# Performance work log

Measured on AMD Instinct MI355X. Metric: run time of the kernel, lower is better.

## Reference

```python
import jax, jax.numpy as jnp
import numpy as np

N, E, D = 100000, 1600000, 64
L = 3          # num_layers
EPS = 1e-5     # LayerNorm eps


def setup_inputs() -> dict:
    key = jax.random.key(0)
    ks = jax.random.split(key, 8)
    s = 0.05
    return {
        "x": jax.random.normal(ks[0], (N, D), jnp.float32),
        "edge_src": jax.random.randint(ks[1], (E,), 0, N, jnp.int32),
        "edge_dst": jax.random.randint(ks[2], (E,), 0, N, jnp.int32),
        # SAGEConv: lin_l (on aggregated neighbors, with bias), lin_r (root, no bias)
        "w_l": (jax.random.normal(ks[3], (L, D, D)) * s).astype(jnp.float32),
        "b_l": jnp.zeros((L, D), jnp.float32),
        "w_r": (jax.random.normal(ks[4], (L, D, D)) * s).astype(jnp.float32),
        # LayerNorm affine params per layer
        "gamma": jnp.ones((L, D), jnp.float32),
        "beta": jnp.zeros((L, D), jnp.float32),
        # residual projection (layer 0 only; Identity afterwards)
        "w_res": (jax.random.normal(ks[5], (D, D)) * s).astype(jnp.float32),
        "b_res": jnp.zeros((D,), jnp.float32),
        # final fc
        "w_fc": (jax.random.normal(ks[6], (D, D)) * s).astype(jnp.float32),
        "b_fc": jnp.zeros((D,), jnp.float32),
    }


def _layer_norm(h, g, b):
    mu = jnp.mean(h, axis=-1, keepdims=True)
    var = jnp.var(h, axis=-1, keepdims=True)
    return (h - mu) * jax.lax.rsqrt(var + EPS) * g + b


def reference(x, edge_src, edge_dst, w_l, b_l, w_r, gamma, beta, w_res, b_res, w_fc, b_fc):
    n = x.shape[0]
    # in-degree for mean aggregation (nodes with no in-edges get 0 aggregate)
    deg = jax.ops.segment_sum(jnp.ones(edge_dst.shape, x.dtype), edge_dst, num_segments=n)
    inv_deg = jnp.where(deg > 0, 1.0 / jnp.maximum(deg, 1.0), 0.0)[:, None]  # [N,1]
    for i in range(L):
        residual = x @ w_res + b_res if i == 0 else x
        # SAGEConv mean aggregation: gather source feats, scatter-sum at dst, divide by degree
        agg = jax.ops.segment_sum(x[edge_src], edge_dst, num_segments=n) * inv_deg  # [N,D]
        h = agg @ w_l[i] + b_l[i] + x @ w_r[i]
        h = jax.nn.relu(_layer_norm(h, gamma[i], beta[i]))
        # dropout is inactive in eval mode
        x = h + residual
    return x @ w_fc + b_fc
```

## Files before the change

### kernel.cpp

```cpp
#include <hip/hip_runtime.h>

typedef unsigned short u16;
typedef __bf16 bf16x8 __attribute__((ext_vector_type(8)));
typedef float f32x4 __attribute__((ext_vector_type(4)));

#define D 64
#define LPITCH 136
#define CHUNKS 256
#define BSHIFT 9

__device__ __forceinline__ float b2f(u16 u) {
    unsigned v = ((unsigned)u) << 16;
    float f;
    __builtin_memcpy(&f, &v, 4);
    return f;
}
__device__ __forceinline__ float u2f_lo(unsigned u) {
    unsigned v = u << 16;
    float f;
    __builtin_memcpy(&f, &v, 4);
    return f;
}
__device__ __forceinline__ float u2f_hi(unsigned u) {
    unsigned v = u & 0xFFFF0000u;
    float f;
    __builtin_memcpy(&f, &v, 4);
    return f;
}
__device__ __forceinline__ u16 f2b(float f) {
    unsigned u;
    __builtin_memcpy(&u, &f, 4);
    u = u + 0x7FFFu + ((u >> 16) & 1u);
    return (u16)(u >> 16);
}
__device__ __forceinline__ bf16x8 ld_frag(const u16* p) {
    union { uint4 u; bf16x8 b; } cv;
    cv.u = *(const uint4*)p;
    return cv.b;
}

__global__ __launch_bounds__(256) void binA_kernel(const int* __restrict__ dst, int E,
                                                   int* __restrict__ H,
                                                   int nbuck, int eper) {
    __shared__ int hist[256];
    int t = threadIdx.x;
    int c = blockIdx.x;
    hist[t] = 0;
    __syncthreads();
    int beg = c * eper;
    int end = min(beg + eper, E);
    for (int i = beg + t; i < end; i += 256) {
        atomicAdd(&hist[dst[i] >> BSHIFT], 1);
    }
    __syncthreads();
    if (t < nbuck) H[c * nbuck + t] = hist[t];
}

__global__ __launch_bounds__(256) void binS2_kernel(const int* __restrict__ H,
                                                    int* __restrict__ Orel,
                                                    int* __restrict__ T,
                                                    int nbuck) {
    __shared__ int ss[256];
    int b = blockIdx.x;
    int t = threadIdx.x;
    int h = H[t * nbuck + b];
    ss[t] = h;
    __syncthreads();
    for (int off = 1; off < 256; off <<= 1) {
        int v = (t >= off) ? ss[t - off] : 0;
        __syncthreads();
        ss[t] += v;
        __syncthreads();
    }
    Orel[t * nbuck + b] = ss[t] - h;
    if (t == 255) T[b] = ss[255];
}

__global__ __launch_bounds__(256) void binT_kernel(const int* __restrict__ T, int nbuck,
                                                   int* __restrict__ base,
                                                   int* __restrict__ row_ptr, int N) {
    __shared__ int sm[256];
    int t = threadIdx.x;
    int v = (t < nbuck) ? T[t] : 0;
    sm[t] = v;
    __syncthreads();
    for (int off = 1; off < 256; off <<= 1) {
        int u = (t >= off) ? sm[t - off] : 0;
        __syncthreads();
        sm[t] += u;
        __syncthreads();
    }
    if (t < nbuck) base[t] = sm[t] - v;
    if (t == 255) {
        base[nbuck] = sm[255];
        row_ptr[N] = sm[255];
    }
}

__global__ __launch_bounds__(256) void binB_kernel(const int* __restrict__ src,
                                                   const int* __restrict__ dst, int E,
                                                   const int* __restrict__ base,
                                                   const int* __restrict__ Orel,
                                                   int* __restrict__ staging,
                                                   int nbuck, int eper) {
    __shared__ int pos[256];
    int t = threadIdx.x;
    int c = blockIdx.x;
    if (t < nbuck) pos[t] = base[t] + Orel[c * nbuck + t];
    __syncthreads();
    int beg = c * eper;
    int end = min(beg + eper, E);
    const int mask = (1 << BSHIFT) - 1;
    for (int i = beg + t; i < end; i += 256) {
        int d = dst[i];
        int b = d >> BSHIFT;
        int p = atomicAdd(&pos[b], 1);
        staging[p] = src[i] | ((d & mask) << 17);
    }
}

__global__ __launch_bounds__(256) void binC_kernel(const int* __restrict__ staging,
                                                   const int* __restrict__ base,
                                                   int* __restrict__ row_ptr,
                                                   float* __restrict__ inv_deg,
                                                   int* __restrict__ col, int N) {
    __shared__ int cnt[512];
    __shared__ int lrp[512];
    __shared__ int sm[256];
    int b = blockIdx.x;
    int t = threadIdx.x;
    int node0 = b << BSHIFT;
    int nn = min(1 << BSHIFT, N - node0);
    cnt[t] = 0;
    cnt[t + 256] = 0;
    __syncthreads();
    int sbeg = base[b], send = base[b + 1];
    for (int i = sbeg + t; i < send; i += 256) {
        atomicAdd(&cnt[staging[i] >> 17], 1);
    }
    __syncthreads();
    int c0 = cnt[2 * t], c1 = cnt[2 * t + 1];
    sm[t] = c0 + c1;
    __syncthreads();
    for (int off = 1; off < 256; off <<= 1) {
        int v = (t >= off) ? sm[t - off] : 0;
        __syncthreads();
        sm[t] += v;
        __syncthreads();
    }
    int excl = sm[t] - c0 - c1;
    lrp[2 * t] = excl;
    lrp[2 * t + 1] = excl + c0;
    __syncthreads();
    for (int i = t; i < nn; i += 256) {
        row_ptr[node0 + i] = sbeg + lrp[i];
        int dd = cnt[i];
        inv_deg[node0 + i] = dd > 0 ? 1.0f / (float)dd : 0.0f;
    }
    __syncthreads();
    for (int i = sbeg + t; i < send; i += 256) {
        int word = staging[i];
        int ld = word >> 17;
        int k = atomicSub(&cnt[ld], 1) - 1;
        col[sbeg + lrp[ld] + k] = word & 0x1FFFF;
    }
}

__global__ __launch_bounds__(256) void cvtprep_kernel(const float* __restrict__ xf,
                                                      u16* __restrict__ xb, int total4,
                                                      const float* __restrict__ wl,
                                                      const float* __restrict__ wr,
                                                      const float* __restrict__ wres,
                                                      const float* __restrict__ wfc,
                                                      u16* __restrict__ WtL,
                                                      u16* __restrict__ WresT,
                                                      u16* __restrict__ WfcT) {
    int gid = blockIdx.x * 256 + threadIdx.x;
    int gstr = gridDim.x * 256;
    for (int i = gid; i < total4; i += gstr) {
        float4 v = *(const float4*)(xf + i * 4);
        ushort4 o;
        o.x = f2b(v.x); o.y = f2b(v.y); o.z = f2b(v.z); o.w = f2b(v.w);
        *(ushort4*)(xb + i * 4) = o;
    }
    for (int idx = gid; idx < 3 * 64 * 128; idx += gstr) {
        int l = idx >> 13;
        int rem = idx & 8191;
        int n = rem >> 7;
        int k = rem & 127;
        float v = (k < 64) ? wl[l * 4096 + k * 64 + n] : wr[l * 4096 + (k - 64) * 64 + n];
        WtL[idx] = f2b(v);
    }
    for (int idx = gid; idx < 4096; idx += gstr) {
        int n = idx >> 6, k = idx & 63;
        WresT[idx] = f2b(wres[k * 64 + n]);
        WfcT[idx] = f2b(wfc[k * 64 + n]);
    }
}

__global__ __launch_bounds__(256, 4) void layer_kernel(const u16* __restrict__ xb_in,
                                                       const int* __restrict__ row_ptr,
                                                       const int* __restrict__ col,
                                                       const float* __restrict__ inv_deg,
                                                       const u16* __restrict__ Wt,
                                                       const float* __restrict__ bl,
                                                       const float* __restrict__ gam,
                                                       const float* __restrict__ bet,
                                                       const u16* __restrict__ WresT,
                                                       const float* __restrict__ bres,
                                                       const u16* __restrict__ WfcT,
                                                       const float* __restrict__ bfc,
                                                       u16* __restrict__ xb_out,
                                                       float* __restrict__ fout,
                                                       int N, int layer0, int final_) {
    __shared__ __align__(16) u16 sA[64 * LPITCH];
    __shared__ __align__(16) u16 sB[64 * LPITCH];
    int tid = threadIdx.x;
    int base = blockIdx.x * 64;
    int lane = tid & 63;
    int w = tid >> 6;

#pragma unroll
    for (int i = 0; i < 4; i++) {
        int idx = i * 256 + tid;
        int r = idx >> 4, c = idx & 15;
        *(uint4*)&sB[r * LPITCH + c * 8] = *(const uint4*)(Wt + idx * 8);
    }
#pragma unroll
    for (int i = 0; i < 2; i++) {
        int idx = i * 256 + tid;
        int r = idx >> 3, c = idx & 7;
        int node = base + r;
        uint4 v = make_uint4(0, 0, 0, 0);
        if (node < N) v = *(const uint4*)(xb_in + node * D + c * 8);
        *(uint4*)&sA[r * LPITCH + 64 + c * 8] = v;
    }

    int slot = lane >> 3;
    int chunk = lane & 7;
#pragma unroll
    for (int r = 0; r < 2; r++) {
        int node_l = w * 16 + r * 8 + slot;
        int node = base + node_l;
        float a0 = 0, a1 = 0, a2 = 0, a3 = 0, a4 = 0, a5 = 0, a6 = 0, a7 = 0;
        uint4 o = make_uint4(0, 0, 0, 0);
        if (node < N) {
            int e = row_ptr[node], end = row_ptr[node + 1];
#define ACC(v)                                          \
    a0 += u2f_lo(v.x); a1 += u2f_hi(v.x);               \
    a2 += u2f_lo(v.y); a3 += u2f_hi(v.y);               \
    a4 += u2f_lo(v.z); a5 += u2f_hi(v.z);               \
    a6 += u2f_lo(v.w); a7 += u2f_hi(v.w);
            for (; e + 7 < end; e += 8) {
                int s0 = col[e],     s1 = col[e + 1], s2 = col[e + 2], s3 = col[e + 3];
                int s4 = col[e + 4], s5 = col[e + 5], s6 = col[e + 6], s7 = col[e + 7];
                uint4 v0 = *(const uint4*)(xb_in + s0 * D + chunk * 8);
                uint4 v1 = *(const uint4*)(xb_in + s1 * D + chunk * 8);
                uint4 v2 = *(const uint4*)(xb_in + s2 * D + chunk * 8);
                uint4 v3 = *(const uint4*)(xb_in + s3 * D + chunk * 8);
                uint4 v4 = *(const uint4*)(xb_in + s4 * D + chunk * 8);
                uint4 v5 = *(const uint4*)(xb_in + s5 * D + chunk * 8);
                uint4 v6 = *(const uint4*)(xb_in + s6 * D + chunk * 8);
                uint4 v7 = *(const uint4*)(xb_in + s7 * D + chunk * 8);
                ACC(v0) ACC(v1) ACC(v2) ACC(v3)
                ACC(v4) ACC(v5) ACC(v6) ACC(v7)
            }
            if (e + 3 < end) {
                int s0 = col[e], s1 = col[e + 1], s2 = col[e + 2], s3 = col[e + 3];
                uint4 v0 = *(const uint4*)(xb_in + s0 * D + chunk * 8);
                uint4 v1 = *(const uint4*)(xb_in + s1 * D + chunk * 8);
                uint4 v2 = *(const uint4*)(xb_in + s2 * D + chunk * 8);
                uint4 v3 = *(const uint4*)(xb_in + s3 * D + chunk * 8);
                ACC(v0) ACC(v1) ACC(v2) ACC(v3)
                e += 4;
            }
            if (e + 1 < end) {
                int s0 = col[e], s1 = col[e + 1];
                uint4 v0 = *(const uint4*)(xb_in + s0 * D + chunk * 8);
                uint4 v1 = *(const uint4*)(xb_in + s1 * D + chunk * 8);
                ACC(v0) ACC(v1)
                e += 2;
            }
            if (e < end) {
                int s0 = col[e];
                uint4 v0 = *(const uint4*)(xb_in + s0 * D + chunk * 8);
                ACC(v0)
            }
#undef ACC
            float m = inv_deg[node];
            o.x = (unsigned)f2b(a0 * m) | ((unsigned)f2b(a1 * m) << 16);
            o.y = (unsigned)f2b(a2 * m) | ((unsigned)f2b(a3 * m) << 16);
            o.z = (unsigned)f2b(a4 * m) | ((unsigned)f2b(a5 * m) << 16);
            o.w = (unsigned)f2b(a6 * m) | ((unsigned)f2b(a7 * m) << 16);
        }
        *(uint4*)&sA[node_l * LPITCH + chunk * 8] = o;
    }
    __syncthreads();

    int q = lane >> 4;
    int ln = lane & 15;
    f32x4 acc[4] = {{0, 0, 0, 0}, {0, 0, 0, 0}, {0, 0, 0, 0}, {0, 0, 0, 0}};
    f32x4 accr[4] = {{0, 0, 0, 0}, {0, 0, 0, 0}, {0, 0, 0, 0}, {0, 0, 0, 0}};
    const u16* aRow = &sA[(w * 16 + ln) * LPITCH];

#pragma unroll
    for (int c = 0; c < 4; c++) {
        bf16x8 a = ld_frag(&aRow[c * 32 + q * 8]);
#pragma unroll
        for (int t = 0; t < 4; t++) {
            bf16x8 b = ld_frag(&sB[(t * 16 + ln) * LPITCH + c * 32 + q * 8]);
            acc[t] = __builtin_amdgcn_mfma_f32_16x16x32_bf16(a, b, acc[t], 0, 0, 0);
        }
    }
    if (layer0) {
#pragma unroll
        for (int c = 0; c < 2; c++) {
            bf16x8 a = ld_frag(&aRow[64 + c * 32 + q * 8]);
#pragma unroll
            for (int t = 0; t < 4; t++) {
                bf16x8 b = ld_frag(WresT + (t * 16 + ln) * 64 + c * 32 + q * 8);
                accr[t] = __builtin_amdgcn_mfma_f32_16x16x32_bf16(a, b, accr[t], 0, 0, 0);
            }
        }
    }

    float bcol[4], gcol[4], btcol[4], brcol[4];
#pragma unroll
    for (int t = 0; t < 4; t++) {
        int colI = t * 16 + ln;
        bcol[t] = bl[colI];
        gcol[t] = gam[colI];
        btcol[t] = bet[colI];
        brcol[t] = layer0 ? bres[colI] : 0.f;
    }
#pragma unroll
    for (int t = 0; t < 4; t++)
#pragma unroll
        for (int r = 0; r < 4; r++) acc[t][r] += bcol[t];

    float ps[4], pq[4];
#pragma unroll
    for (int r = 0; r < 4; r++) {
        float s = 0, s2 = 0;
#pragma unroll
        for (int t = 0; t < 4; t++) { float h = acc[t][r]; s += h; s2 += h * h; }
        ps[r] = s; pq[r] = s2;
    }
    for (int off = 1; off < 16; off <<= 1) {
#pragma unroll
        for (int r = 0; r < 4; r++) {
            ps[r] += __shfl_xor(ps[r], off, 64);
            pq[r] += __shfl_xor(pq[r], off, 64);
        }
    }
#pragma unroll
    for (int r = 0; r < 4; r++) {
        int nb = w * 16 + q * 4 + r;
        float mu = ps[r] * (1.f / 64.f);
        float var = pq[r] * (1.f / 64.f) - mu * mu;
        var = var < 0.f ? 0.f : var;
        float rstd = rsqrtf(var + 1e-5f);
#pragma unroll
        for (int t = 0; t < 4; t++) {
            int colI = t * 16 + ln;
            float hn = (acc[t][r] - mu) * rstd * gcol[t] + btcol[t];
            hn = hn > 0.f ? hn : 0.f;
            float res = layer0 ? (accr[t][r] + brcol[t])
                               : b2f(sA[nb * LPITCH + 64 + colI]);
            sA[nb * LPITCH + colI] = f2b(hn + res);
        }
    }

    if (final_) {
        f32x4 accf[4] = {{0, 0, 0, 0}, {0, 0, 0, 0}, {0, 0, 0, 0}, {0, 0, 0, 0}};
#pragma unroll
        for (int c = 0; c < 2; c++) {
            bf16x8 a = ld_frag(&aRow[c * 32 + q * 8]);
#pragma unroll
            for (int t = 0; t < 4; t++) {
                bf16x8 b = ld_frag(WfcT + (t * 16 + ln) * 64 + c * 32 + q * 8);
                accf[t] = __builtin_amdgcn_mfma_f32_16x16x32_bf16(a, b, accf[t], 0, 0, 0);
            }
        }
#pragma unroll
        for (int r = 0; r < 4; r++) {
            int node = base + w * 16 + q * 4 + r;
            if (node >= N) continue;
#pragma unroll
            for (int t = 0; t < 4; t++) {
                int colI = t * 16 + ln;
                fout[node * D + colI] = accf[t][r] + bfc[colI];
            }
        }
    } else {
#pragma unroll
        for (int i = 0; i < 2; i++) {
            int idx = i * 64 + lane;
            int row = w * 16 + (idx >> 3);
            int ch = idx & 7;
            int node = base + row;
            if (node < N)
                *(uint4*)(xb_out + node * D + ch * 8) = *(const uint4*)&sA[row * LPITCH + ch * 8];
        }
    }
}

extern "C" void kernel_launch(void* const* d_in, const int* in_sizes, int n_in,
                              void* d_out, int out_size, void* d_ws, size_t ws_size,
                              hipStream_t stream) {
    const float* x_in = (const float*)d_in[0];
    const int* e_src = (const int*)d_in[1];
    const int* e_dst = (const int*)d_in[2];
    const float* w_l = (const float*)d_in[3];
    const float* b_l = (const float*)d_in[4];
    const float* w_r = (const float*)d_in[5];
    const float* gam = (const float*)d_in[6];
    const float* bet = (const float*)d_in[7];
    const float* w_res = (const float*)d_in[8];
    const float* b_res = (const float*)d_in[9];
    const float* w_fc = (const float*)d_in[10];
    const float* b_fc = (const float*)d_in[11];
    float* out = (float*)d_out;

    const int N = in_sizes[0] / D;
    const int E = in_sizes[1];
    const int nbuck = ((N - 1) >> BSHIFT) + 1;
    const int eper = (E + CHUNKS - 1) / CHUNKS;

    size_t o = 0;
    auto carve = [&](size_t bytes) {
        size_t cur = o;
        o += (bytes + 255) & ~(size_t)255;
        return (char*)d_ws + cur;
    };
    int* row_ptr = (int*)carve((size_t)(N + 1) * 4);
    float* inv_deg = (float*)carve((size_t)N * 4);
    int* colA = (int*)carve((size_t)E * 4);
    int* staging = (int*)carve((size_t)E * 4);
    int* Hh = (int*)carve((size_t)CHUNKS * nbuck * 4);
    int* Orel = (int*)carve((size_t)CHUNKS * nbuck * 4);
    int* Tb = (int*)carve((size_t)nbuck * 4);
    int* baseB = (int*)carve((size_t)(nbuck + 1) * 4);
    u16* WtL = (u16*)carve(3 * 64 * 128 * 2);
    u16* WresT = (u16*)carve(64 * 64 * 2);
    u16* WfcT = (u16*)carve(64 * 64 * 2);
    u16* xbA = (u16*)carve((size_t)N * D * 2);
    u16* xbB = (u16*)carve((size_t)N * D * 2);

    binA_kernel<<<CHUNKS, 256, 0, stream>>>(e_dst, E, Hh, nbuck, eper);
    binS2_kernel<<<nbuck, 256, 0, stream>>>(Hh, Orel, Tb, nbuck);
    binT_kernel<<<1, 256, 0, stream>>>(Tb, nbuck, baseB, row_ptr, N);
    binB_kernel<<<CHUNKS, 256, 0, stream>>>(e_src, e_dst, E, baseB, Orel, staging, nbuck, eper);
    binC_kernel<<<nbuck, 256, 0, stream>>>(staging, baseB, row_ptr, inv_deg, colA, N);

    cvtprep_kernel<<<1024, 256, 0, stream>>>(x_in, xbA, N * D / 4,
                                             w_l, w_r, w_res, w_fc, WtL, WresT, WfcT);

    int gridT = (N + 63) / 64;

    layer_kernel<<<gridT, 256, 0, stream>>>(xbA, row_ptr, colA, inv_deg, WtL,
                                            b_l, gam, bet, WresT, b_res,
                                            WfcT, b_fc, xbB, out, N, 1, 0);
    layer_kernel<<<gridT, 256, 0, stream>>>(xbB, row_ptr, colA, inv_deg, WtL + 8192,
                                            b_l + 64, gam + 64, bet + 64, WresT, b_res,
                                            WfcT, b_fc, xbA, out, N, 0, 0);
    layer_kernel<<<gridT, 256, 0, stream>>>(xbA, row_ptr, colA, inv_deg, WtL + 16384,
                                            b_l + 128, gam + 128, bet + 128, WresT, b_res,
                                            WfcT, b_fc, xbB, out, N, 0, 1);
}
```

Before: 282.5 us.

## Use 128-node tiles with 512 threads and dynamic LDS work queue for aggregation

Doubles the layer kernel tile to 128 nodes with 512 threads. Gather-aggregation slots now pull node indices from an LDS atomic counter, which balances uneven degrees across wavefronts. Row pointers and inverse degrees are staged in LDS first. The costs are an extra barrier, per-node atomics, and higher LDS use per block, which may limit occupancy.

```diff
diff --git a/kernel.cpp b/kernel.cpp
--- a/kernel.cpp
+++ b/kernel.cpp
@@ -6,6 +6,7 @@
 
 #define D 64
 #define LPITCH 136
+#define TILE 128
 #define CHUNKS 256
 #define BSHIFT 9
 
@@ -198,7 +199,7 @@
     }
 }
 
-__global__ __launch_bounds__(256, 4) void layer_kernel(const u16* __restrict__ xb_in,
+__global__ __launch_bounds__(512, 6) void layer_kernel(const u16* __restrict__ xb_in,
                                                        const int* __restrict__ row_ptr,
                                                        const int* __restrict__ col,
                                                        const float* __restrict__ inv_deg,
@@ -213,39 +214,50 @@
                                                        u16* __restrict__ xb_out,
                                                        float* __restrict__ fout,
                                                        int N, int layer0, int final_) {
-    __shared__ __align__(16) u16 sA[64 * LPITCH];
+    __shared__ __align__(16) u16 sA[TILE * LPITCH];
     __shared__ __align__(16) u16 sB[64 * LPITCH];
+    __shared__ int rp[TILE + 1];
+    __shared__ float ideg[TILE];
+    __shared__ int ctr;
     int tid = threadIdx.x;
-    int base = blockIdx.x * 64;
+    int base = blockIdx.x * TILE;
     int lane = tid & 63;
     int w = tid >> 6;
 
 #pragma unroll
-    for (int i = 0; i < 4; i++) {
-        int idx = i * 256 + tid;
+    for (int i = 0; i < 2; i++) {
+        int idx = i * 512 + tid;
         int r = idx >> 4, c = idx & 15;
         *(uint4*)&sB[r * LPITCH + c * 8] = *(const uint4*)(Wt + idx * 8);
     }
 #pragma unroll
     for (int i = 0; i < 2; i++) {
-        int idx = i * 256 + tid;
+        int idx = i * 512 + tid;
         int r = idx >> 3, c = idx & 7;
         int node = base + r;
         uint4 v = make_uint4(0, 0, 0, 0);
         if (node < N) v = *(const uint4*)(xb_in + node * D + c * 8);
         *(uint4*)&sA[r * LPITCH + 64 + c * 8] = v;
     }
-
-    int slot = lane >> 3;
+    if (tid <= TILE) {
+        int node = base + tid;
+        rp[tid] = (node <= N) ? row_ptr[node] : 0;
+        if (tid < TILE) ideg[tid] = (node < N) ? inv_deg[node] : 0.f;
+    }
+    if (tid == 0) ctr = 0;
+    __syncthreads();
+
     int chunk = lane & 7;
-#pragma unroll
-    for (int r = 0; r < 2; r++) {
-        int node_l = w * 16 + r * 8 + slot;
-        int node = base + node_l;
+    for (;;) {
+        int j = 0;
+        if ((lane & 7) == 0) j = atomicAdd(&ctr, 1);
+        j = __shfl(j, lane & 56, 64);
+        if (j >= TILE) break;
+        int node = base + j;
         float a0 = 0, a1 = 0, a2 = 0, a3 = 0, a4 = 0, a5 = 0, a6 = 0, a7 = 0;
         uint4 o = make_uint4(0, 0, 0, 0);
         if (node < N) {
-            int e = row_ptr[node], end = row_ptr[node + 1];
+            int e = rp[j], end = rp[j + 1];
 #define ACC(v)                                          \
     a0 += u2f_lo(v.x); a1 += u2f_hi(v.x);               \
     a2 += u2f_lo(v.y); a3 += u2f_hi(v.y);               \
@@ -287,13 +299,13 @@
                 ACC(v0)
             }
 #undef ACC
-            float m = inv_deg[node];
+            float m = ideg[j];
             o.x = (unsigned)f2b(a0 * m) | ((unsigned)f2b(a1 * m) << 16);
             o.y = (unsigned)f2b(a2 * m) | ((unsigned)f2b(a3 * m) << 16);
             o.z = (unsigned)f2b(a4 * m) | ((unsigned)f2b(a5 * m) << 16);
             o.w = (unsigned)f2b(a6 * m) | ((unsigned)f2b(a7 * m) << 16);
         }
-        *(uint4*)&sA[node_l * LPITCH + chunk * 8] = o;
+        *(uint4*)&sA[j * LPITCH + chunk * 8] = o;
     }
     __syncthreads();
 
@@ -456,15 +468,15 @@
     cvtprep_kernel<<<1024, 256, 0, stream>>>(x_in, xbA, N * D / 4,
                                              w_l, w_r, w_res, w_fc, WtL, WresT, WfcT);
 
-    int gridT = (N + 63) / 64;
-
-    layer_kernel<<<gridT, 256, 0, stream>>>(xbA, row_ptr, colA, inv_deg, WtL,
+    int gridT = (N + TILE - 1) / TILE;
+
+    layer_kernel<<<gridT, 512, 0, stream>>>(xbA, row_ptr, colA, inv_deg, WtL,
                                             b_l, gam, bet, WresT, b_res,
                                             WfcT, b_fc, xbB, out, N, 1, 0);
-    layer_kernel<<<gridT, 256, 0, stream>>>(xbB, row_ptr, colA, inv_deg, WtL + 8192,
+    layer_kernel<<<gridT, 512, 0, stream>>>(xbB, row_ptr, colA, inv_deg, WtL + 8192,
                                             b_l + 64, gam + 64, bet + 64, WresT, b_res,
                                             WfcT, b_fc, xbA, out, N, 0, 0);
-    layer_kernel<<<gridT, 256, 0, stream>>>(xbA, row_ptr, colA, inv_deg, WtL + 16384,
+    layer_kernel<<<gridT, 512, 0, stream>>>(xbA, row_ptr, colA, inv_deg, WtL + 16384,
                                             b_l + 128, gam + 128, bet + 128, WresT, b_res,
                                             WfcT, b_fc, xbB, out, N, 0, 1);
 }
```

Measured after the change: 318.8 us. +12.8%, slower.

## Merge CSR build and conversion kernels into one cooperative kernel

Applied to the files above, without the earlier changes.

Replaces the five CSR-binning kernels and the bf16 conversion kernel with a single cooperative launch of 256 blocks, using grid.sync() between phases. This removes five kernel launch boundaries and their drain/fill gaps, and lets the x/weight conversion run on the same grid after bucket sorting. In exchange it adds grid-wide barriers, and the conversion now runs on 256 blocks instead of 1024 and only after the CSR phases complete.

```diff
diff --git a/kernel.cpp b/kernel.cpp
--- a/kernel.cpp
+++ b/kernel.cpp
@@ -1,4 +1,7 @@
 #include <hip/hip_runtime.h>
+#include <hip/hip_cooperative_groups.h>
+
+namespace cg = cooperative_groups;
 
 typedef unsigned short u16;
 typedef __bf16 bf16x8 __attribute__((ext_vector_type(8)));
@@ -39,162 +42,156 @@
     return cv.b;
 }
 
-__global__ __launch_bounds__(256) void binA_kernel(const int* __restrict__ dst, int E,
-                                                   int* __restrict__ H,
-                                                   int nbuck, int eper) {
-    __shared__ int hist[256];
+struct CsrArgs {
+    const int* dst;
+    const int* src;
+    int E, N, nbuck, eper, total4;
+    int* H;
+    int* Orel;
+    int* T;
+    int* base;
+    int* row_ptr;
+    float* inv_deg;
+    int* staging;
+    int* col;
+    const float* xf;
+    const float* wl;
+    const float* wr;
+    const float* wres;
+    const float* wfc;
+    u16* xb;
+    u16* WtL;
+    u16* WresT;
+    u16* WfcT;
+};
+
+__global__ __launch_bounds__(256) void csr_kernel(CsrArgs a) {
+    __shared__ union {
+        int hist[256];
+        struct { int cnt[512]; int lrp[512]; int sm[256]; } c;
+    } sh;
+    cg::grid_group grid = cg::this_grid();
     int t = threadIdx.x;
     int c = blockIdx.x;
-    hist[t] = 0;
+
+    sh.hist[t] = 0;
     __syncthreads();
-    int beg = c * eper;
-    int end = min(beg + eper, E);
-    for (int i = beg + t; i < end; i += 256) {
-        atomicAdd(&hist[dst[i] >> BSHIFT], 1);
+    {
+        int beg = c * a.eper, end = min(beg + a.eper, a.E);
+        for (int i = beg + t; i < end; i += 256)
+            atomicAdd(&sh.hist[a.dst[i] >> BSHIFT], 1);
     }
     __syncthreads();
-    if (t < nbuck) H[c * nbuck + t] = hist[t];
-}
-
-__global__ __launch_bounds__(256) void binS2_kernel(const int* __restrict__ H,
-                                                    int* __restrict__ Orel,
-                                                    int* __restrict__ T,
-                                                    int nbuck) {
-    __shared__ int ss[256];
-    int b = blockIdx.x;
-    int t = threadIdx.x;
-    int h = H[t * nbuck + b];
-    ss[t] = h;
-    __syncthreads();
-    for (int off = 1; off < 256; off <<= 1) {
-        int v = (t >= off) ? ss[t - off] : 0;
-        __syncthreads();
-        ss[t] += v;
-        __syncthreads();
-    }
-    Orel[t * nbuck + b] = ss[t] - h;
-    if (t == 255) T[b] = ss[255];
-}
-
-__global__ __launch_bounds__(256) void binT_kernel(const int* __restrict__ T, int nbuck,
-                                                   int* __restrict__ base,
-                                                   int* __restrict__ row_ptr, int N) {
-    __shared__ int sm[256];
-    int t = threadIdx.x;
-    int v = (t < nbuck) ? T[t] : 0;
-    sm[t] = v;
-    __syncthreads();
-    for (int off = 1; off < 256; off <<= 1) {
-        int u = (t >= off) ? sm[t - off] : 0;
-        __syncthreads();
-        sm[t] += u;
-        __syncthreads();
-    }
-    if (t < nbuck) base[t] = sm[t] - v;
-    if (t == 255) {
-        base[nbuck] = sm[255];
-        row_ptr[N] = sm[255];
-    }
-}
-
-__global__ __launch_bounds__(256) void binB_kernel(const int* __restrict__ src,
-                                                   const int* __restrict__ dst, int E,
-                                                   const int* __restrict__ base,
-                                                   const int* __restrict__ Orel,
-                                                   int* __restrict__ staging,
-                                                   int nbuck, int eper) {
-    __shared__ int pos[256];
-    int t = threadIdx.x;
-    int c = blockIdx.x;
-    if (t < nbuck) pos[t] = base[t] + Orel[c * nbuck + t];
-    __syncthreads();
-    int beg = c * eper;
-    int end = min(beg + eper, E);
-    const int mask = (1 << BSHIFT) - 1;
-    for (int i = beg + t; i < end; i += 256) {
-        int d = dst[i];
-        int b = d >> BSHIFT;
-        int p = atomicAdd(&pos[b], 1);
-        staging[p] = src[i] | ((d & mask) << 17);
-    }
-}
-
-__global__ __launch_bounds__(256) void binC_kernel(const int* __restrict__ staging,
-                                                   const int* __restrict__ base,
-                                                   int* __restrict__ row_ptr,
-                                                   float* __restrict__ inv_deg,
-                                                   int* __restrict__ col, int N) {
-    __shared__ int cnt[512];
-    __shared__ int lrp[512];
-    __shared__ int sm[256];
-    int b = blockIdx.x;
-    int t = threadIdx.x;
-    int node0 = b << BSHIFT;
-    int nn = min(1 << BSHIFT, N - node0);
-    cnt[t] = 0;
-    cnt[t + 256] = 0;
-    __syncthreads();
-    int sbeg = base[b], send = base[b + 1];
-    for (int i = sbeg + t; i < send; i += 256) {
-        atomicAdd(&cnt[staging[i] >> 17], 1);
-    }
-    __syncthreads();
-    int c0 = cnt[2 * t], c1 = cnt[2 * t + 1];
-    sm[t] = c0 + c1;
-    __syncthreads();
-    for (int off = 1; off < 256; off <<= 1) {
-        int v = (t >= off) ? sm[t - off] : 0;
-        __syncthreads();
-        sm[t] += v;
-        __syncthreads();
-    }
-    int excl = sm[t] - c0 - c1;
-    lrp[2 * t] = excl;
-    lrp[2 * t + 1] = excl + c0;
-    __syncthreads();
-    for (int i = t; i < nn; i += 256) {
-        row_ptr[node0 + i] = sbeg + lrp[i];
-        int dd = cnt[i];
-        inv_deg[node0 + i] = dd > 0 ? 1.0f / (float)dd : 0.0f;
-    }
-    __syncthreads();
-    for (int i = sbeg + t; i < send; i += 256) {
-        int word = staging[i];
-        int ld = word >> 17;
-        int k = atomicSub(&cnt[ld], 1) - 1;
-        col[sbeg + lrp[ld] + k] = word & 0x1FFFF;
-    }
-}
-
-__global__ __launch_bounds__(256) void cvtprep_kernel(const float* __restrict__ xf,
-                                                      u16* __restrict__ xb, int total4,
-                                                      const float* __restrict__ wl,
-                                                      const float* __restrict__ wr,
-                                                      const float* __restrict__ wres,
-                                                      const float* __restrict__ wfc,
-                                                      u16* __restrict__ WtL,
-                                                      u16* __restrict__ WresT,
-                                                      u16* __restrict__ WfcT) {
-    int gid = blockIdx.x * 256 + threadIdx.x;
-    int gstr = gridDim.x * 256;
-    for (int i = gid; i < total4; i += gstr) {
-        float4 v = *(const float4*)(xf + i * 4);
-        ushort4 o;
-        o.x = f2b(v.x); o.y = f2b(v.y); o.z = f2b(v.z); o.w = f2b(v.w);
-        *(ushort4*)(xb + i * 4) = o;
-    }
-    for (int idx = gid; idx < 3 * 64 * 128; idx += gstr) {
-        int l = idx >> 13;
-        int rem = idx & 8191;
-        int n = rem >> 7;
-        int k = rem & 127;
-        float v = (k < 64) ? wl[l * 4096 + k * 64 + n] : wr[l * 4096 + (k - 64) * 64 + n];
-        WtL[idx] = f2b(v);
-    }
-    for (int idx = gid; idx < 4096; idx += gstr) {
-        int n = idx >> 6, k = idx & 63;
-        WresT[idx] = f2b(wres[k * 64 + n]);
-        WfcT[idx] = f2b(wfc[k * 64 + n]);
+    if (t < a.nbuck) a.H[c * a.nbuck + t] = sh.hist[t];
+    grid.sync();
+
+    if (c < a.nbuck) {
+        int h = a.H[t * a.nbuck + c];
+        sh.hist[t] = h;
+        __syncthreads();
+        for (int off = 1; off < 256; off <<= 1) {
+            int v = (t >= off) ? sh.hist[t - off] : 0;
+            __syncthreads();
+            sh.hist[t] += v;
+            __syncthreads();
+        }
+        a.Orel[t * a.nbuck + c] = sh.hist[t] - h;
+        if (t == 255) a.T[c] = sh.hist[255];
+    }
+    grid.sync();
+
+    if (c == 0) {
+        int v = (t < a.nbuck) ? a.T[t] : 0;
+        sh.hist[t] = v;
+        __syncthreads();
+        for (int off = 1; off < 256; off <<= 1) {
+            int u = (t >= off) ? sh.hist[t - off] : 0;
+            __syncthreads();
+            sh.hist[t] += u;
+            __syncthreads();
+        }
+        if (t < a.nbuck) a.base[t] = sh.hist[t] - v;
+        if (t == 255) {
+            a.base[a.nbuck] = sh.hist[255];
+            a.row_ptr[a.N] = sh.hist[255];
+        }
+    }
+    grid.sync();
+
+    {
+        if (t < a.nbuck) sh.hist[t] = a.base[t] + a.Orel[c * a.nbuck + t];
+        __syncthreads();
+        int beg = c * a.eper, end = min(beg + a.eper, a.E);
+        const int mask = (1 << BSHIFT) - 1;
+        for (int i = beg + t; i < end; i += 256) {
+            int d = a.dst[i];
+            int b = d >> BSHIFT;
+            int p = atomicAdd(&sh.hist[b], 1);
+            a.staging[p] = a.src[i] | ((d & mask) << 17);
+        }
+    }
+    grid.sync();
+
+    if (c < a.nbuck) {
+        int node0 = c << BSHIFT;
+        int nn = min(1 << BSHIFT, a.N - node0);
+        sh.c.cnt[t] = 0;
+        sh.c.cnt[t + 256] = 0;
+        __syncthreads();
+        int sbeg = a.base[c], send = a.base[c + 1];
+        for (int i = sbeg + t; i < send; i += 256)
+            atomicAdd(&sh.c.cnt[a.staging[i] >> 17], 1);
+        __syncthreads();
+        int c0 = sh.c.cnt[2 * t], c1 = sh.c.cnt[2 * t + 1];
+        sh.c.sm[t] = c0 + c1;
+        __syncthreads();
+        for (int off = 1; off < 256; off <<= 1) {
+            int v = (t >= off) ? sh.c.sm[t - off] : 0;
+            __syncthreads();
+            sh.c.sm[t] += v;
+            __syncthreads();
+        }
+        int excl = sh.c.sm[t] - c0 - c1;
+        sh.c.lrp[2 * t] = excl;
+        sh.c.lrp[2 * t + 1] = excl + c0;
+        __syncthreads();
+        for (int i = t; i < nn; i += 256) {
+            a.row_ptr[node0 + i] = sbeg + sh.c.lrp[i];
+            int dd = sh.c.cnt[i];
+            a.inv_deg[node0 + i] = dd > 0 ? 1.0f / (float)dd : 0.0f;
+        }
+        __syncthreads();
+        for (int i = sbeg + t; i < send; i += 256) {
+            int word = a.staging[i];
+            int ld = word >> 17;
+            int k = atomicSub(&sh.c.cnt[ld], 1) - 1;
+            a.col[sbeg + sh.c.lrp[ld] + k] = word & 0x1FFFF;
+        }
+    }
+
+    {
+        int gid = c * 256 + t;
+        int gstr = 256 * 256;
+        for (int i = gid; i < a.total4; i += gstr) {
+            float4 v = *(const float4*)(a.xf + i * 4);
+            ushort4 o;
+            o.x = f2b(v.x); o.y = f2b(v.y); o.z = f2b(v.z); o.w = f2b(v.w);
+            *(ushort4*)(a.xb + i * 4) = o;
+        }
+        for (int idx = gid; idx < 3 * 64 * 128; idx += gstr) {
+            int l = idx >> 13;
+            int rem = idx & 8191;
+            int n = rem >> 7;
+            int k = rem & 127;
+            float v = (k < 64) ? a.wl[l * 4096 + k * 64 + n]
+                               : a.wr[l * 4096 + (k - 64) * 64 + n];
+            a.WtL[idx] = f2b(v);
+        }
+        for (int idx = gid; idx < 4096; idx += gstr) {
+            int n = idx >> 6, k = idx & 63;
+            a.WresT[idx] = f2b(a.wres[k * 64 + n]);
+            a.WfcT[idx] = f2b(a.wfc[k * 64 + n]);
+        }
     }
 }
 
@@ -447,14 +444,34 @@
     u16* xbA = (u16*)carve((size_t)N * D * 2);
     u16* xbB = (u16*)carve((size_t)N * D * 2);
 
-    binA_kernel<<<CHUNKS, 256, 0, stream>>>(e_dst, E, Hh, nbuck, eper);
-    binS2_kernel<<<nbuck, 256, 0, stream>>>(Hh, Orel, Tb, nbuck);
-    binT_kernel<<<1, 256, 0, stream>>>(Tb, nbuck, baseB, row_ptr, N);
-    binB_kernel<<<CHUNKS, 256, 0, stream>>>(e_src, e_dst, E, baseB, Orel, staging, nbuck, eper);
-    binC_kernel<<<nbuck, 256, 0, stream>>>(staging, baseB, row_ptr, inv_deg, colA, N);
-
-    cvtprep_kernel<<<1024, 256, 0, stream>>>(x_in, xbA, N * D / 4,
-                                             w_l, w_r, w_res, w_fc, WtL, WresT, WfcT);
+    CsrArgs args;
+    args.dst = e_dst;
+    args.src = e_src;
+    args.E = E;
+    args.N = N;
+    args.nbuck = nbuck;
+    args.eper = eper;
+    args.total4 = N * D / 4;
+    args.H = Hh;
+    args.Orel = Orel;
+    args.T = Tb;
+    args.base = baseB;
+    args.row_ptr = row_ptr;
+    args.inv_deg = inv_deg;
+    args.staging = staging;
+    args.col = colA;
+    args.xf = x_in;
+    args.wl = w_l;
+    args.wr = w_r;
+    args.wres = w_res;
+    args.wfc = w_fc;
+    args.xb = xbA;
+    args.WtL = WtL;
+    args.WresT = WresT;
+    args.WfcT = WfcT;
+    void* kargs[] = {&args};
+    hipLaunchCooperativeKernel((const void*)csr_kernel, dim3(CHUNKS), dim3(256),
+                               kargs, 0, stream);
 
     int gridT = (N + 63) / 64;
 
```

After: 435.2 us. 54.1% more time.

## Fuse preprocessing kernels, stage tile column indices in LDS, coalesce final output stores

Applied to the files above, without the earlier changes.

Folds the bf16 conversion and weight transposes into the histogram kernel, and removes the single-block bucket scan kernel by recomputing the bucket prefix sum inside binB and binC. This cuts two launches from the preprocessing chain. The layer kernel now caches the tile's row pointers, inverse degrees and (when they fit in 1280 entries) column indices in LDS. The final FC output is staged through shared memory so it can be written as coalesced float4 stores. In exchange it adds LDS usage (which may reduce occupancy), a redundant scan in every block, and an extra barrier.

```diff
diff --git a/kernel.cpp b/kernel.cpp
--- a/kernel.cpp
+++ b/kernel.cpp
@@ -8,6 +8,7 @@
 #define LPITCH 136
 #define CHUNKS 256
 #define BSHIFT 9
+#define CCAP 1280
 
 __device__ __forceinline__ float b2f(u16 u) {
     unsigned v = ((unsigned)u) << 16;
@@ -40,20 +41,52 @@
 }
 
 __global__ __launch_bounds__(256) void binA_kernel(const int* __restrict__ dst, int E,
-                                                   int* __restrict__ H,
-                                                   int nbuck, int eper) {
+                                                   int* __restrict__ H, int nbuck, int eper,
+                                                   const float* __restrict__ xf,
+                                                   u16* __restrict__ xb, int total4,
+                                                   const float* __restrict__ wl,
+                                                   const float* __restrict__ wr,
+                                                   const float* __restrict__ wres,
+                                                   const float* __restrict__ wfc,
+                                                   u16* __restrict__ WtL,
+                                                   u16* __restrict__ WresT,
+                                                   u16* __restrict__ WfcT,
+                                                   int* __restrict__ row_ptr, int N) {
     __shared__ int hist[256];
     int t = threadIdx.x;
     int c = blockIdx.x;
     hist[t] = 0;
     __syncthreads();
-    int beg = c * eper;
-    int end = min(beg + eper, E);
-    for (int i = beg + t; i < end; i += 256) {
-        atomicAdd(&hist[dst[i] >> BSHIFT], 1);
+    {
+        int beg = c * eper, end = min(beg + eper, E);
+        for (int i = beg + t; i < end; i += 256)
+            atomicAdd(&hist[dst[i] >> BSHIFT], 1);
     }
     __syncthreads();
     if (t < nbuck) H[c * nbuck + t] = hist[t];
+
+    int gid = c * 256 + t;
+    int gstr = CHUNKS * 256;
+    if (gid == 0) row_ptr[N] = E;
+    for (int i = gid; i < total4; i += gstr) {
+        float4 v = *(const float4*)(xf + i * 4);
+        ushort4 o;
+        o.x = f2b(v.x); o.y = f2b(v.y); o.z = f2b(v.z); o.w = f2b(v.w);
+        *(ushort4*)(xb + i * 4) = o;
+    }
+    for (int idx = gid; idx < 3 * 64 * 128; idx += gstr) {
+        int l = idx >> 13;
+        int rem = idx & 8191;
+        int n = rem >> 7;
+        int k = rem & 127;
+        float v = (k < 64) ? wl[l * 4096 + k * 64 + n] : wr[l * 4096 + (k - 64) * 64 + n];
+        WtL[idx] = f2b(v);
+    }
+    for (int idx = gid; idx < 4096; idx += gstr) {
+        int n = idx >> 6, k = idx & 63;
+        WresT[idx] = f2b(wres[k * 64 + n]);
+        WfcT[idx] = f2b(wfc[k * 64 + n]);
+    }
 }
 
 __global__ __launch_bounds__(256) void binS2_kernel(const int* __restrict__ H,
@@ -76,76 +109,76 @@
     if (t == 255) T[b] = ss[255];
 }
 
-__global__ __launch_bounds__(256) void binT_kernel(const int* __restrict__ T, int nbuck,
-                                                   int* __restrict__ base,
-                                                   int* __restrict__ row_ptr, int N) {
-    __shared__ int sm[256];
-    int t = threadIdx.x;
-    int v = (t < nbuck) ? T[t] : 0;
-    sm[t] = v;
-    __syncthreads();
-    for (int off = 1; off < 256; off <<= 1) {
-        int u = (t >= off) ? sm[t - off] : 0;
-        __syncthreads();
-        sm[t] += u;
-        __syncthreads();
-    }
-    if (t < nbuck) base[t] = sm[t] - v;
-    if (t == 255) {
-        base[nbuck] = sm[255];
-        row_ptr[N] = sm[255];
-    }
-}
-
 __global__ __launch_bounds__(256) void binB_kernel(const int* __restrict__ src,
                                                    const int* __restrict__ dst, int E,
-                                                   const int* __restrict__ base,
+                                                   const int* __restrict__ T,
                                                    const int* __restrict__ Orel,
                                                    int* __restrict__ staging,
                                                    int nbuck, int eper) {
-    __shared__ int pos[256];
+    __shared__ int sc[256];
     int t = threadIdx.x;
     int c = blockIdx.x;
-    if (t < nbuck) pos[t] = base[t] + Orel[c * nbuck + t];
-    __syncthreads();
-    int beg = c * eper;
-    int end = min(beg + eper, E);
+    int v = (t < nbuck) ? T[t] : 0;
+    sc[t] = v;
+    __syncthreads();
+    for (int off = 1; off < 256; off <<= 1) {
+        int u = (t >= off) ? sc[t - off] : 0;
+        __syncthreads();
+        sc[t] += u;
+        __syncthreads();
+    }
+    int baseT = sc[t] - v;
+    int porel = (t < nbuck) ? Orel[c * nbuck + t] : 0;
+    __syncthreads();
+    sc[t] = baseT + porel;
+    __syncthreads();
+    int beg = c * eper, end = min(beg + eper, E);
     const int mask = (1 << BSHIFT) - 1;
     for (int i = beg + t; i < end; i += 256) {
         int d = dst[i];
         int b = d >> BSHIFT;
-        int p = atomicAdd(&pos[b], 1);
+        int p = atomicAdd(&sc[b], 1);
         staging[p] = src[i] | ((d & mask) << 17);
     }
 }
 
 __global__ __launch_bounds__(256) void binC_kernel(const int* __restrict__ staging,
-                                                   const int* __restrict__ base,
+                                                   const int* __restrict__ T,
                                                    int* __restrict__ row_ptr,
                                                    float* __restrict__ inv_deg,
-                                                   int* __restrict__ col, int N) {
+                                                   int* __restrict__ col, int N, int nbuck) {
     __shared__ int cnt[512];
     __shared__ int lrp[512];
     __shared__ int sm[256];
+    __shared__ int span[2];
     int b = blockIdx.x;
     int t = threadIdx.x;
+    int v = (t < nbuck) ? T[t] : 0;
+    sm[t] = v;
+    __syncthreads();
+    for (int off = 1; off < 256; off <<= 1) {
+        int u = (t >= off) ? sm[t - off] : 0;
+        __syncthreads();
+        sm[t] += u;
+        __syncthreads();
+    }
+    if (t == b) { span[0] = sm[t] - v; span[1] = sm[t]; }
+    cnt[t] = 0;
+    cnt[t + 256] = 0;
+    __syncthreads();
+    int sbeg = span[0], send = span[1];
     int node0 = b << BSHIFT;
     int nn = min(1 << BSHIFT, N - node0);
-    cnt[t] = 0;
-    cnt[t + 256] = 0;
-    __syncthreads();
-    int sbeg = base[b], send = base[b + 1];
-    for (int i = sbeg + t; i < send; i += 256) {
+    for (int i = sbeg + t; i < send; i += 256)
         atomicAdd(&cnt[staging[i] >> 17], 1);
-    }
     __syncthreads();
     int c0 = cnt[2 * t], c1 = cnt[2 * t + 1];
     sm[t] = c0 + c1;
     __syncthreads();
     for (int off = 1; off < 256; off <<= 1) {
-        int v = (t >= off) ? sm[t - off] : 0;
-        __syncthreads();
-        sm[t] += v;
+        int u = (t >= off) ? sm[t - off] : 0;
+        __syncthreads();
+        sm[t] += u;
         __syncthreads();
     }
     int excl = sm[t] - c0 - c1;
@@ -163,38 +196,6 @@
         int ld = word >> 17;
         int k = atomicSub(&cnt[ld], 1) - 1;
         col[sbeg + lrp[ld] + k] = word & 0x1FFFF;
-    }
-}
-
-__global__ __launch_bounds__(256) void cvtprep_kernel(const float* __restrict__ xf,
-                                                      u16* __restrict__ xb, int total4,
-                                                      const float* __restrict__ wl,
-                                                      const float* __restrict__ wr,
-                                                      const float* __restrict__ wres,
-                                                      const float* __restrict__ wfc,
-                                                      u16* __restrict__ WtL,
-                                                      u16* __restrict__ WresT,
-                                                      u16* __restrict__ WfcT) {
-    int gid = blockIdx.x * 256 + threadIdx.x;
-    int gstr = gridDim.x * 256;
-    for (int i = gid; i < total4; i += gstr) {
-        float4 v = *(const float4*)(xf + i * 4);
-        ushort4 o;
-        o.x = f2b(v.x); o.y = f2b(v.y); o.z = f2b(v.z); o.w = f2b(v.w);
-        *(ushort4*)(xb + i * 4) = o;
-    }
-    for (int idx = gid; idx < 3 * 64 * 128; idx += gstr) {
-        int l = idx >> 13;
-        int rem = idx & 8191;
-        int n = rem >> 7;
-        int k = rem & 127;
-        float v = (k < 64) ? wl[l * 4096 + k * 64 + n] : wr[l * 4096 + (k - 64) * 64 + n];
-        WtL[idx] = f2b(v);
-    }
-    for (int idx = gid; idx < 4096; idx += gstr) {
-        int n = idx >> 6, k = idx & 63;
-        WresT[idx] = f2b(wres[k * 64 + n]);
-        WfcT[idx] = f2b(wfc[k * 64 + n]);
     }
 }
 
@@ -215,6 +216,9 @@
                                                        int N, int layer0, int final_) {
     __shared__ __align__(16) u16 sA[64 * LPITCH];
     __shared__ __align__(16) u16 sB[64 * LPITCH];
+    __shared__ int lcol[CCAP];
+    __shared__ int rp[65];
+    __shared__ float ideg[64];
     int tid = threadIdx.x;
     int base = blockIdx.x * 64;
     int lane = tid & 63;
@@ -235,25 +239,34 @@
         if (node < N) v = *(const uint4*)(xb_in + node * D + c * 8);
         *(uint4*)&sA[r * LPITCH + 64 + c * 8] = v;
     }
+    if (tid < 65) rp[tid] = row_ptr[min(base + tid, N)];
+    if (tid < 64) ideg[tid] = (base + tid < N) ? inv_deg[base + tid] : 0.f;
+    __syncthreads();
+
+    int e0 = rp[0];
+    int tileE = rp[64] - e0;
+    bool fits = tileE <= CCAP;
+    if (fits) {
+        for (int i = tid; i < tileE; i += 256) lcol[i] = col[e0 + i];
+    }
+    __syncthreads();
 
     int slot = lane >> 3;
     int chunk = lane & 7;
-#pragma unroll
-    for (int r = 0; r < 2; r++) {
-        int node_l = w * 16 + r * 8 + slot;
-        int node = base + node_l;
-        float a0 = 0, a1 = 0, a2 = 0, a3 = 0, a4 = 0, a5 = 0, a6 = 0, a7 = 0;
-        uint4 o = make_uint4(0, 0, 0, 0);
-        if (node < N) {
-            int e = row_ptr[node], end = row_ptr[node + 1];
+    auto run_gather = [&](auto LD) {
+#pragma unroll
+        for (int r = 0; r < 2; r++) {
+            int node_l = w * 16 + r * 8 + slot;
+            float a0 = 0, a1 = 0, a2 = 0, a3 = 0, a4 = 0, a5 = 0, a6 = 0, a7 = 0;
+            int e = rp[node_l], end = rp[node_l + 1];
 #define ACC(v)                                          \
     a0 += u2f_lo(v.x); a1 += u2f_hi(v.x);               \
     a2 += u2f_lo(v.y); a3 += u2f_hi(v.y);               \
     a4 += u2f_lo(v.z); a5 += u2f_hi(v.z);               \
     a6 += u2f_lo(v.w); a7 += u2f_hi(v.w);
             for (; e + 7 < end; e += 8) {
-                int s0 = col[e],     s1 = col[e + 1], s2 = col[e + 2], s3 = col[e + 3];
-                int s4 = col[e + 4], s5 = col[e + 5], s6 = col[e + 6], s7 = col[e + 7];
+                int s0 = LD(e),     s1 = LD(e + 1), s2 = LD(e + 2), s3 = LD(e + 3);
+                int s4 = LD(e + 4), s5 = LD(e + 5), s6 = LD(e + 6), s7 = LD(e + 7);
                 uint4 v0 = *(const uint4*)(xb_in + s0 * D + chunk * 8);
                 uint4 v1 = *(const uint4*)(xb_in + s1 * D + chunk * 8);
                 uint4 v2 = *(const uint4*)(xb_in + s2 * D + chunk * 8);
@@ -266,7 +279,7 @@
                 ACC(v4) ACC(v5) ACC(v6) ACC(v7)
             }
             if (e + 3 < end) {
-                int s0 = col[e], s1 = col[e + 1], s2 = col[e + 2], s3 = col[e + 3];
+                int s0 = LD(e), s1 = LD(e + 1), s2 = LD(e + 2), s3 = LD(e + 3);
                 uint4 v0 = *(const uint4*)(xb_in + s0 * D + chunk * 8);
                 uint4 v1 = *(const uint4*)(xb_in + s1 * D + chunk * 8);
                 uint4 v2 = *(const uint4*)(xb_in + s2 * D + chunk * 8);
@@ -275,26 +288,29 @@
                 e += 4;
             }
             if (e + 1 < end) {
-                int s0 = col[e], s1 = col[e + 1];
+                int s0 = LD(e), s1 = LD(e + 1);
                 uint4 v0 = *(const uint4*)(xb_in + s0 * D + chunk * 8);
                 uint4 v1 = *(const uint4*)(xb_in + s1 * D + chunk * 8);
                 ACC(v0) ACC(v1)
                 e += 2;
             }
             if (e < end) {
-                int s0 = col[e];
+                int s0 = LD(e);
                 uint4 v0 = *(const uint4*)(xb_in + s0 * D + chunk * 8);
                 ACC(v0)
             }
 #undef ACC
-            float m = inv_deg[node];
+            float m = ideg[node_l];
+            uint4 o;
             o.x = (unsigned)f2b(a0 * m) | ((unsigned)f2b(a1 * m) << 16);
             o.y = (unsigned)f2b(a2 * m) | ((unsigned)f2b(a3 * m) << 16);
             o.z = (unsigned)f2b(a4 * m) | ((unsigned)f2b(a5 * m) << 16);
             o.w = (unsigned)f2b(a6 * m) | ((unsigned)f2b(a7 * m) << 16);
-        }
-        *(uint4*)&sA[node_l * LPITCH + chunk * 8] = o;
-    }
+            *(uint4*)&sA[node_l * LPITCH + chunk * 8] = o;
+        }
+    };
+    if (fits) run_gather([&](int e) { return lcol[e - e0]; });
+    else      run_gather([&](int e) { return col[e]; });
     __syncthreads();
 
     int q = lane >> 4;
@@ -382,15 +398,25 @@
                 accf[t] = __builtin_amdgcn_mfma_f32_16x16x32_bf16(a, b, accf[t], 0, 0, 0);
             }
         }
+        __syncthreads();
+        float* fB = (float*)sB;
 #pragma unroll
         for (int r = 0; r < 4; r++) {
-            int node = base + w * 16 + q * 4 + r;
-            if (node >= N) continue;
+            int nb = w * 16 + q * 4 + r;
 #pragma unroll
             for (int t = 0; t < 4; t++) {
                 int colI = t * 16 + ln;
-                fout[node * D + colI] = accf[t][r] + bfc[colI];
-            }
+                fB[nb * 68 + colI] = accf[t][r] + bfc[colI];
+            }
+        }
+        __syncthreads();
+#pragma unroll
+        for (int i = 0; i < 4; i++) {
+            int idx = i * 256 + tid;
+            int row = idx >> 4, cc = idx & 15;
+            int node = base + row;
+            if (node < N)
+                *(float4*)(fout + node * D + cc * 4) = *(const float4*)&fB[row * 68 + cc * 4];
         }
     } else {
 #pragma unroll
@@ -440,21 +466,20 @@
     int* Hh = (int*)carve((size_t)CHUNKS * nbuck * 4);
     int* Orel = (int*)carve((size_t)CHUNKS * nbuck * 4);
     int* Tb = (int*)carve((size_t)nbuck * 4);
-    int* baseB = (int*)carve((size_t)(nbuck + 1) * 4);
     u16* WtL = (u16*)carve(3 * 64 * 128 * 2);
     u16* WresT = (u16*)carve(64 * 64 * 2);
     u16* WfcT = (u16*)carve(64 * 64 * 2);
     u16* xbA = (u16*)carve((size_t)N * D * 2);
     u16* xbB = (u16*)carve((size_t)N * D * 2);
 
-    binA_kernel<<<CHUNKS, 256, 0, stream>>>(e_dst, E, Hh, nbuck, eper);
+    binA_kernel<<<CHUNKS, 256, 0, stream>>>(e_dst, E, Hh, nbuck, eper,
+                                            x_in, xbA, N * D / 4,
+                                            w_l, w_r, w_res, w_fc, WtL, WresT, WfcT,
+                                            row_ptr, N);
     binS2_kernel<<<nbuck, 256, 0, stream>>>(Hh, Orel, Tb, nbuck);
-    binT_kernel<<<1, 256, 0, stream>>>(Tb, nbuck, baseB, row_ptr, N);
-    binB_kernel<<<CHUNKS, 256, 0, stream>>>(e_src, e_dst, E, baseB, Orel, staging, nbuck, eper);
-    binC_kernel<<<nbuck, 256, 0, stream>>>(staging, baseB, row_ptr, inv_deg, colA, N);
-
-    cvtprep_kernel<<<1024, 256, 0, stream>>>(x_in, xbA, N * D / 4,
-                                             w_l, w_r, w_res, w_fc, WtL, WresT, WfcT);
+    binB_kernel<<<CHUNKS, 256, 0, stream>>>(e_src, e_dst, E, Tb, Orel, staging,
+                                            nbuck, eper);
+    binC_kernel<<<nbuck, 256, 0, stream>>>(staging, Tb, row_ptr, inv_deg, colA, N, nbuck);
 
     int gridT = (N + 63) / 64;
 
```

Result: no change. 281.1 us (-0.5%).
